# Kernel tuning notes

Hardware: AMD Instinct MI355X
Metric: run time of the kernel (lower is better)

The kernel has to match this reference:

```python
import jax, jax.numpy as jnp
import numpy as np


def setup_inputs() -> dict:
    key = jax.random.key(0)
    T, B, D, H = 512, 64, 512, 512
    k0, k1, k2, k3 = jax.random.split(key, 4)
    x = jax.random.normal(k0, (T, B, D), dtype=jnp.float32)
    # packed-sequence lengths, descending (as PackedSequence requires), at least T//2
    lengths = jnp.sort(jax.random.randint(k1, (B,), T // 2, T + 1))[::-1].astype(jnp.int64)
    s = 1.0 / np.sqrt(H)
    # gates stacked in order (i, f, c, o): same math as 8 separate per-gate linears
    Wx = jax.random.normal(k2, (4 * H, D), dtype=jnp.float32) * s
    Wh = jax.random.normal(k3, (4 * H, H), dtype=jnp.float32) * s
    # reset_parameters(): b_i = b_c = b_o = 0, b_f = 1
    b = jnp.concatenate([jnp.zeros(H), jnp.ones(H), jnp.zeros(2 * H)]).astype(jnp.float32)
    return {"x": x, "lengths": lengths, "Wx": Wx, "Wh": Wh, "b": b}


def reference(x, lengths, Wx, Wh, b):
    T, B, D = x.shape
    H = Wh.shape[1]
    # input projections for all timesteps at once (one big GEMM)
    xg = jnp.einsum('tbd,gd->tbg', x, Wx) + b  # [T, B, 4H]
    # validity mask per (t, b): packed recurrence only updates active rows
    mask = (jnp.arange(T)[:, None] < lengths[None, :])[..., None]  # [T, B, 1]

    def step(carry, inp):
        h, c = carry
        xg_t, m = inp
        g = xg_t + h @ Wh.T  # [B, 4H]
        i, f, cc, o = jnp.split(g, 4, axis=-1)
        i = jax.nn.sigmoid(i)
        f = jax.nn.sigmoid(f)
        o = jax.nn.sigmoid(o)
        c_t = f * c + i * jnp.tanh(cc)
        h_t = o * jnp.tanh(c_t)
        c_new = jnp.where(m, c_t, c)
        h_new = jnp.where(m, h_t, h)
        out_t = jnp.where(m, h_new, jnp.zeros((), x.dtype))
        return (h_new, c_new), out_t

    h0 = jnp.zeros((B, H), dtype=x.dtype)
    (h_T, c_T), out = jax.lax.scan(step, (h0, h0), (xg, mask))
    return out  # padded equivalent of the PackedSequence output, [T, B, H]
```

## Files before the change

kernel.cpp:

```cpp
#include <hip/hip_runtime.h>
#include <stdint.h>


#define TT 512
#define BB 64
#define DD 512
#define HH 512
#define NWG 256
#define NTHR 512
#define GR 8

typedef short short8 __attribute__((ext_vector_type(8)));
typedef float f32x4 __attribute__((ext_vector_type(4)));

__device__ __forceinline__ uint16_t bf16_rne(float f) {
  uint32_t u = __float_as_uint(f);
  u += 0x7fffu + ((u >> 16) & 1u);
  return (uint16_t)(u >> 16);
}

__device__ __forceinline__ void split2(float f, uint16_t &hi, uint16_t &lo) {
  uint16_t h = bf16_rne(f);
  hi = h;
  lo = bf16_rne(f - __uint_as_float(((uint32_t)h) << 16));
}

__device__ __forceinline__ float sigf(float v) { return 1.0f / (1.0f + __expf(-v)); }
__device__ __forceinline__ float tanh_(float v) {
  return 1.0f - 2.0f / (__expf(2.0f * v) + 1.0f);
}

__global__ void build_frags(const float* __restrict__ W, uint32_t* __restrict__ frag) {
  const int tid = blockIdx.x * 256 + threadIdx.x;
  const int lane = tid & 63;
  const int ks = (tid >> 6) & 15;
  const int nblk = tid >> 10;
  const int col = nblk * 16 + (lane & 15);
  const int k0 = ks * 32 + ((lane >> 4) << 3);
  const float* src = W + (size_t)col * 512 + k0;
  float4 a = *(const float4*)(src);
  float4 b = *(const float4*)(src + 4);
  float v[8] = {a.x, a.y, a.z, a.w, b.x, b.y, b.z, b.w};
  uint32_t hw[4], lw[4];
#pragma unroll
  for (int j = 0; j < 4; ++j) {
    uint16_t h0, l0, h1, l1;
    split2(v[2 * j], h0, l0);
    split2(v[2 * j + 1], h1, l1);
    hw[j] = (uint32_t)h0 | ((uint32_t)h1 << 16);
    lw[j] = (uint32_t)l0 | ((uint32_t)l1 << 16);
  }
  uint4* dst = (uint4*)(frag + (size_t)tid * 8);
  dst[0] = make_uint4(hw[0], hw[1], hw[2], hw[3]);
  dst[1] = make_uint4(lw[0], lw[1], lw[2], lw[3]);
}

__global__ __launch_bounds__(NTHR, 2) void lstm_main(
    const float* __restrict__ x, const int* __restrict__ len,
    const float* __restrict__ bias, const uint32_t* __restrict__ fragWx,
    const uint32_t* __restrict__ fragWh, uint32_t* __restrict__ h_pair,
    float* __restrict__ out) {
  const int tid = threadIdx.x;
  const int lane = tid & 63;
  const int wave = tid >> 6;
  const int gp = wave >> 1;
  const int kh = wave & 1;
  const int group = blockIdx.x & 7;
  const int jblk = blockIdx.x >> 3;
  const int b0 = group * GR;
  const int j0 = jblk << 4;
  uint32_t* hbase = h_pair + (size_t)group * 2 * (GR * HH);

  __shared__ uint16_t AH[GR * 512];
  __shared__ uint16_t AL[GR * 512];
  __shared__ float ex[8][GR][16];
  __shared__ float c_st[GR][16];
  __shared__ float h_st[GR][16];
  __shared__ float bias_l[4][16];
  __shared__ int len_l[GR];

  if (tid < GR * 16) {
    c_st[tid >> 4][tid & 15] = 0.0f;
    h_st[tid >> 4][tid & 15] = 0.0f;
  }
  if (tid < 64) bias_l[tid >> 4][tid & 15] = bias[(size_t)(tid >> 4) * HH + j0 + (tid & 15)];
  if (tid < GR) len_l[tid] = len[b0 + tid];

  short8 bxh[8], bxl[8], bhh[8], bhl[8];
  {
    const int nblk = gp * 32 + jblk;
#pragma unroll
    for (int ksl = 0; ksl < 8; ++ksl) {
      const size_t idx = ((size_t)(nblk * 16 + kh * 8 + ksl) * 64 + lane) * 8;
      uint4 vh = *(const uint4*)(fragWx + idx);
      uint4 vl = *(const uint4*)(fragWx + idx + 4);
      bxh[ksl] = __builtin_bit_cast(short8, vh);
      bxl[ksl] = __builtin_bit_cast(short8, vl);
      uint4 wh = *(const uint4*)(fragWh + idx);
      uint4 wl = *(const uint4*)(fragWh + idx + 4);
      bhh[ksl] = __builtin_bit_cast(short8, wh);
      bhl[ksl] = __builtin_bit_cast(short8, wl);
    }
  }

  const int arow = lane & 7;
  const int achk = (lane >> 4) << 4;
  const int axr = arow << 4;
  const char* rowH = (const char*)AH + arow * 1024;
  const char* rowL = (const char*)AL + arow * 1024;

  f32x4 hh = {0.f, 0.f, 0.f, 0.f}, lh = {0.f, 0.f, 0.f, 0.f}, hl = {0.f, 0.f, 0.f, 0.f};
  float4 xp[2];

#define LOAD_XP(tt)                                                            \
  _Pragma("unroll") for (int i = 0; i < 2; ++i) {                              \
    const int flat4 = i * 2048 + tid * 4;                                      \
    const int row = flat4 >> 9;                                                \
    const int col = flat4 & 511;                                               \
    xp[i] = *(const float4*)(x + ((size_t)(tt) * BB + b0 + row) * DD + col);   \
  }

#define STAGE_XP()                                                             \
  _Pragma("unroll") for (int i = 0; i < 2; ++i) {                              \
    const int flat4 = i * 2048 + tid * 4;                                      \
    const int row = flat4 >> 9;                                                \
    const int col = flat4 & 511;                                               \
    uint16_t h0, l0, h1, l1, h2, l2, h3, l3;                                   \
    split2(xp[i].x, h0, l0);                                                   \
    split2(xp[i].y, h1, l1);                                                   \
    split2(xp[i].z, h2, l2);                                                   \
    split2(xp[i].w, h3, l3);                                                   \
    const uint32_t hw0 = (uint32_t)h0 | ((uint32_t)h1 << 16);                  \
    const uint32_t hw1 = (uint32_t)h2 | ((uint32_t)h3 << 16);                  \
    const uint32_t lw0 = (uint32_t)l0 | ((uint32_t)l1 << 16);                  \
    const uint32_t lw1 = (uint32_t)l2 | ((uint32_t)l3 << 16);                  \
    const int off = row * 1024 + ((col * 2) ^ (row << 4));                     \
    *(uint2*)((char*)AH + off) = make_uint2(hw0, hw1);                         \
    *(uint2*)((char*)AL + off) = make_uint2(lw0, lw1);                         \
  }

#define X_MFMA()                                                               \
  hh = (f32x4){0.f, 0.f, 0.f, 0.f};                                           \
  lh = (f32x4){0.f, 0.f, 0.f, 0.f};                                           \
  hl = (f32x4){0.f, 0.f, 0.f, 0.f};                                           \
  _Pragma("unroll") for (int ksl = 0; ksl < 8; ++ksl) {                        \
    const int off = ((kh * 8 + ksl) * 64 + achk) ^ axr;                        \
    short8 ah = *(const short8*)(rowH + off);                                  \
    short8 al = *(const short8*)(rowL + off);                                  \
    hh = __builtin_amdgcn_mfma_f32_16x16x32_bf16(ah, bxh[ksl], hh, 0, 0, 0);   \
    lh = __builtin_amdgcn_mfma_f32_16x16x32_bf16(al, bxh[ksl], lh, 0, 0, 0);   \
    hl = __builtin_amdgcn_mfma_f32_16x16x32_bf16(ah, bxl[ksl], hl, 0, 0, 0);   \
  }

  LOAD_XP(0);
  __syncthreads();
  STAGE_XP();
  __syncthreads();
  X_MFMA();
  LOAD_XP(1);

  for (int t = 0; t < TT; ++t) {
    const int rbuf = t & 1;
    const int wbuf = rbuf ^ 1;

    if (t > 0) {
      const uint32_t tagp = (((uint32_t)(t - 1)) >> 1) & 3u;
      const uint32_t EXd = ((tagp & 1u) << 14) | ((tagp >> 1) << 30);
      const uint64_t EX2 = ((uint64_t)EXd << 32) | EXd;
      const uint64_t MK2 = 0x4000400040004000ull;
      const unsigned long long* pb =
          (const unsigned long long*)(hbase + (size_t)rbuf * (GR * HH)) +
          (size_t)tid * 4;
      uint64_t w0, w1, w2, w3;
      for (;;) {
        w0 = __hip_atomic_load(pb + 0, __ATOMIC_RELAXED, __HIP_MEMORY_SCOPE_AGENT);
        w1 = __hip_atomic_load(pb + 1, __ATOMIC_RELAXED, __HIP_MEMORY_SCOPE_AGENT);
        w2 = __hip_atomic_load(pb + 2, __ATOMIC_RELAXED, __HIP_MEMORY_SCOPE_AGENT);
        w3 = __hip_atomic_load(pb + 3, __ATOMIC_RELAXED, __HIP_MEMORY_SCOPE_AGENT);
        const uint64_t bad =
            (((w0 ^ EX2) | (w1 ^ EX2) | (w2 ^ EX2) | (w3 ^ EX2)) & MK2);
        if (bad == 0ull) break;
      }
      __syncthreads();

      {
        const uint32_t CM = ~0x40004000u;
        uint32_t d0 = (uint32_t)w0 & CM, d1 = (uint32_t)(w0 >> 32) & CM;
        uint32_t d2 = (uint32_t)w1 & CM, d3 = (uint32_t)(w1 >> 32) & CM;
        uint32_t d4 = (uint32_t)w2 & CM, d5 = (uint32_t)(w2 >> 32) & CM;
        uint32_t d6 = (uint32_t)w3 & CM, d7 = (uint32_t)(w3 >> 32) & CM;
        const uint32_t hi0 = (d0 & 0xFFFFu) | (d1 << 16);
        const uint32_t lo0 = (d0 >> 16) | (d1 & 0xFFFF0000u);
        const uint32_t hi1 = (d2 & 0xFFFFu) | (d3 << 16);
        const uint32_t lo1 = (d2 >> 16) | (d3 & 0xFFFF0000u);
        const uint32_t hi2 = (d4 & 0xFFFFu) | (d5 << 16);
        const uint32_t lo2 = (d4 >> 16) | (d5 & 0xFFFF0000u);
        const uint32_t hi3 = (d6 & 0xFFFFu) | (d7 << 16);
        const uint32_t lo3 = (d6 >> 16) | (d7 & 0xFFFF0000u);
        const int woff = wave * 1024 + ((lane * 16) ^ (wave << 4));
        *(uint4*)((char*)AH + woff) = make_uint4(hi0, hi1, hi2, hi3);
        *(uint4*)((char*)AL + woff) = make_uint4(lo0, lo1, lo2, lo3);
      }
      __syncthreads();

#pragma unroll
      for (int ksl = 0; ksl < 8; ++ksl) {
        const int off = ((kh * 8 + ksl) * 64 + achk) ^ axr;
        short8 ah = *(const short8*)(rowH + off);
        short8 al = *(const short8*)(rowL + off);
        hh = __builtin_amdgcn_mfma_f32_16x16x32_bf16(ah, bhh[ksl], hh, 0, 0, 0);
        lh = __builtin_amdgcn_mfma_f32_16x16x32_bf16(al, bhh[ksl], lh, 0, 0, 0);
        hl = __builtin_amdgcn_mfma_f32_16x16x32_bf16(ah, bhl[ksl], hl, 0, 0, 0);
      }
    }

    {
      const int crow = (lane >> 4) << 2;
      const int ccol = lane & 15;
      if (crow < GR) {
#pragma unroll
        for (int r = 0; r < 4; ++r) ex[wave][crow + r][ccol] = hh[r] + lh[r] + hl[r];
      }
    }
    __syncthreads();

    if (tid < GR * 16) {
      const int brow = tid >> 4;
      const int jc = tid & 15;
      const float p0 = ex[0][brow][jc] + ex[1][brow][jc] + bias_l[0][jc];
      const float p1 = ex[2][brow][jc] + ex[3][brow][jc] + bias_l[1][jc];
      const float p2 = ex[4][brow][jc] + ex[5][brow][jc] + bias_l[2][jc];
      const float p3 = ex[6][brow][jc] + ex[7][brow][jc] + bias_l[3][jc];
      const float ig = sigf(p0);
      const float fg = sigf(p1);
      const float cc = tanh_(p2);
      const float og = sigf(p3);
      const float co = c_st[brow][jc];
      const float ct = fg * co + ig * cc;
      const float ht = og * tanh_(ct);
      const bool m = (t < len_l[brow]);
      const float cn = m ? ct : co;
      const float hn = m ? ht : h_st[brow][jc];
      c_st[brow][jc] = cn;
      h_st[brow][jc] = hn;
      out[((size_t)t * BB + b0 + brow) * HH + j0 + jc] = m ? ht : 0.0f;
      uint16_t ph, pl;
      split2(hn, ph, pl);
      const uint32_t tagw = (((uint32_t)t) >> 1) & 3u;
      const uint32_t TB = ((tagw & 1u) << 14) | ((tagw >> 1) << 30);
      const uint32_t hv = ((uint32_t)ph | ((uint32_t)pl << 16)) | TB;
      __hip_atomic_store(hbase + (size_t)wbuf * (GR * HH) + brow * HH + j0 + jc,
                         hv, __ATOMIC_RELAXED, __HIP_MEMORY_SCOPE_AGENT);
    }

    if (t + 1 < TT) {
      STAGE_XP();
      __syncthreads();
      X_MFMA();
      LOAD_XP(min(t + 2, TT - 1));
    }
  }
}

extern "C" void kernel_launch(void* const* d_in, const int* in_sizes, int n_in,
                              void* d_out, int out_size, void* d_ws, size_t ws_size,
                              hipStream_t stream) {
  const float* x = (const float*)d_in[0];
  const int* len = (const int*)d_in[1];
  const float* Wx = (const float*)d_in[2];
  const float* Wh = (const float*)d_in[3];
  const float* bias = (const float*)d_in[4];
  float* out = (float*)d_out;

  const size_t FRAG_DW = (size_t)128 * 16 * 64 * 8;
  uint32_t* fragWx = (uint32_t*)d_ws;
  uint32_t* fragWh = fragWx + FRAG_DW;
  uint32_t* h_pair = fragWh + FRAG_DW;

  hipMemsetAsync(h_pair, 0xFF, (size_t)8 * 2 * GR * HH * 4, stream);

  build_frags<<<dim3(512), dim3(256), 0, stream>>>(Wx, fragWx);
  build_frags<<<dim3(512), dim3(256), 0, stream>>>(Wh, fragWh);

  void* args[] = {(void*)&x,      (void*)&len,    (void*)&bias, (void*)&fragWx,
                  (void*)&fragWh, (void*)&h_pair, (void*)&out};
  hipLaunchCooperativeKernel((void*)lstm_main, dim3(NWG), dim3(NTHR), args, 0, stream);
}
```

Before: 1.445 ms.

## Add workgroup-scope local h exchange buffer with fallback to agent-scope polling

Adds a second copy of the hidden-state exchange buffer that producers write with workgroup-scope atomic stores and that consumers poll using atomic fetch_add of zero. The idea is to hit a nearer cache level (same XCD/L2) instead of the agent-scope path. The local poll gets a bounded number of tries. If it never sees the expected tag, that workgroup falls back for good to the original agent-scope polling. This doubles the h stores, adds a memset, and relies on cross-workgroup visibility that workgroup scope does not guarantee, so correctness leans on the fallback.

```diff
diff --git a/kernel.cpp b/kernel.cpp
--- a/kernel.cpp
+++ b/kernel.cpp
@@ -59,7 +59,7 @@
     const float* __restrict__ x, const int* __restrict__ len,
     const float* __restrict__ bias, const uint32_t* __restrict__ fragWx,
     const uint32_t* __restrict__ fragWh, uint32_t* __restrict__ h_pair,
-    float* __restrict__ out) {
+    uint32_t* __restrict__ h_loc, float* __restrict__ out) {
   const int tid = threadIdx.x;
   const int lane = tid & 63;
   const int wave = tid >> 6;
@@ -70,6 +70,7 @@
   const int b0 = group * GR;
   const int j0 = jblk << 4;
   uint32_t* hbase = h_pair + (size_t)group * 2 * (GR * HH);
+  uint32_t* lbase = h_loc + (size_t)group * 2 * (GR * HH);
 
   __shared__ uint16_t AH[GR * 512];
   __shared__ uint16_t AL[GR * 512];
@@ -111,6 +112,7 @@
 
   f32x4 hh = {0.f, 0.f, 0.f, 0.f}, lh = {0.f, 0.f, 0.f, 0.f}, hl = {0.f, 0.f, 0.f, 0.f};
   float4 xp[2];
+  bool use_local = true;
 
 #define LOAD_XP(tt)                                                            \
   _Pragma("unroll") for (int i = 0; i < 2; ++i) {                              \
@@ -168,18 +170,42 @@
       const uint32_t EXd = ((tagp & 1u) << 14) | ((tagp >> 1) << 30);
       const uint64_t EX2 = ((uint64_t)EXd << 32) | EXd;
       const uint64_t MK2 = 0x4000400040004000ull;
-      const unsigned long long* pb =
-          (const unsigned long long*)(hbase + (size_t)rbuf * (GR * HH)) +
-          (size_t)tid * 4;
       uint64_t w0, w1, w2, w3;
-      for (;;) {
-        w0 = __hip_atomic_load(pb + 0, __ATOMIC_RELAXED, __HIP_MEMORY_SCOPE_AGENT);
-        w1 = __hip_atomic_load(pb + 1, __ATOMIC_RELAXED, __HIP_MEMORY_SCOPE_AGENT);
-        w2 = __hip_atomic_load(pb + 2, __ATOMIC_RELAXED, __HIP_MEMORY_SCOPE_AGENT);
-        w3 = __hip_atomic_load(pb + 3, __ATOMIC_RELAXED, __HIP_MEMORY_SCOPE_AGENT);
-        const uint64_t bad =
-            (((w0 ^ EX2) | (w1 ^ EX2) | (w2 ^ EX2) | (w3 ^ EX2)) & MK2);
-        if (bad == 0ull) break;
+      bool got = false;
+
+      if (use_local) {
+        unsigned long long* lp =
+            (unsigned long long*)(lbase + (size_t)rbuf * (GR * HH)) +
+            (size_t)tid * 4;
+        int tries = (t == 1) ? 256 : 16;
+        do {
+          w0 = __hip_atomic_fetch_add(lp + 0, 0ull, __ATOMIC_RELAXED,
+                                      __HIP_MEMORY_SCOPE_WORKGROUP);
+          w1 = __hip_atomic_fetch_add(lp + 1, 0ull, __ATOMIC_RELAXED,
+                                      __HIP_MEMORY_SCOPE_WORKGROUP);
+          w2 = __hip_atomic_fetch_add(lp + 2, 0ull, __ATOMIC_RELAXED,
+                                      __HIP_MEMORY_SCOPE_WORKGROUP);
+          w3 = __hip_atomic_fetch_add(lp + 3, 0ull, __ATOMIC_RELAXED,
+                                      __HIP_MEMORY_SCOPE_WORKGROUP);
+          got = ((((w0 ^ EX2) | (w1 ^ EX2) | (w2 ^ EX2) | (w3 ^ EX2)) & MK2) ==
+                 0ull);
+        } while (!got && --tries);
+        if (!got) use_local = false;
+      }
+
+      if (!got) {
+        const unsigned long long* pb =
+            (const unsigned long long*)(hbase + (size_t)rbuf * (GR * HH)) +
+            (size_t)tid * 4;
+        for (;;) {
+          w0 = __hip_atomic_load(pb + 0, __ATOMIC_RELAXED, __HIP_MEMORY_SCOPE_AGENT);
+          w1 = __hip_atomic_load(pb + 1, __ATOMIC_RELAXED, __HIP_MEMORY_SCOPE_AGENT);
+          w2 = __hip_atomic_load(pb + 2, __ATOMIC_RELAXED, __HIP_MEMORY_SCOPE_AGENT);
+          w3 = __hip_atomic_load(pb + 3, __ATOMIC_RELAXED, __HIP_MEMORY_SCOPE_AGENT);
+          const uint64_t bad =
+              (((w0 ^ EX2) | (w1 ^ EX2) | (w2 ^ EX2) | (w3 ^ EX2)) & MK2);
+          if (bad == 0ull) break;
+        }
       }
       __syncthreads();
 
@@ -249,8 +275,11 @@
       const uint32_t tagw = (((uint32_t)t) >> 1) & 3u;
       const uint32_t TB = ((tagw & 1u) << 14) | ((tagw >> 1) << 30);
       const uint32_t hv = ((uint32_t)ph | ((uint32_t)pl << 16)) | TB;
-      __hip_atomic_store(hbase + (size_t)wbuf * (GR * HH) + brow * HH + j0 + jc,
-                         hv, __ATOMIC_RELAXED, __HIP_MEMORY_SCOPE_AGENT);
+      const size_t eoff = (size_t)wbuf * (GR * HH) + brow * HH + j0 + jc;
+      __hip_atomic_store(lbase + eoff, hv, __ATOMIC_RELAXED,
+                         __HIP_MEMORY_SCOPE_WORKGROUP);
+      __hip_atomic_store(hbase + eoff, hv, __ATOMIC_RELAXED,
+                         __HIP_MEMORY_SCOPE_AGENT);
     }
 
     if (t + 1 < TT) {
@@ -273,16 +302,19 @@
   float* out = (float*)d_out;
 
   const size_t FRAG_DW = (size_t)128 * 16 * 64 * 8;
+  const size_t HP_DW = (size_t)8 * 2 * GR * HH;
   uint32_t* fragWx = (uint32_t*)d_ws;
   uint32_t* fragWh = fragWx + FRAG_DW;
   uint32_t* h_pair = fragWh + FRAG_DW;
-
-  hipMemsetAsync(h_pair, 0xFF, (size_t)8 * 2 * GR * HH * 4, stream);
+  uint32_t* h_loc = h_pair + HP_DW;
+
+  hipMemsetAsync(h_pair, 0xFF, HP_DW * 4, stream);
+  hipMemsetAsync(h_loc, 0xFF, HP_DW * 4, stream);
 
   build_frags<<<dim3(512), dim3(256), 0, stream>>>(Wx, fragWx);
   build_frags<<<dim3(512), dim3(256), 0, stream>>>(Wh, fragWh);
 
-  void* args[] = {(void*)&x,      (void*)&len,    (void*)&bias, (void*)&fragWx,
-                  (void*)&fragWh, (void*)&h_pair, (void*)&out};
+  void* args[] = {(void*)&x,      (void*)&len,   (void*)&bias, (void*)&fragWx,
+                  (void*)&fragWh, (void*)&h_pair, (void*)&h_loc, (void*)&out};
   hipLaunchCooperativeKernel((void*)lstm_main, dim3(NWG), dim3(NTHR), args, 0, stream);
 }
```

Measured after the change: 1.585 ms. 1.1x slower.

## Hoist input projection into separate GEMM kernel and halve recurrent workgroups

Applied to the files above, without the earlier changes.

Moves the x·Wx input projection out of the serial recurrence into a separate parallel GEMM kernel that writes a [T,B,4H] fp32 buffer to workspace. The recurrent kernel then only does the h·Wh MFMAs and prefetches the precomputed gate inputs, with 16 batch rows per group across 128 workgroups instead of 8 rows across 256. This takes work off the latency-bound critical path and reduces the number of communicating workgroups. In exchange it needs an extra 256MB-class workspace write/read, and falls back to the old kernel if the workspace is too small.

```diff
diff --git a/kernel.cpp b/kernel.cpp
--- a/kernel.cpp
+++ b/kernel.cpp
@@ -6,9 +6,11 @@
 #define BB 64
 #define DD 512
 #define HH 512
-#define NWG 256
 #define NTHR 512
-#define GR 8
+#define NWG2 128
+#define GR2 16
+#define NWG4 256
+#define GR4 8
 
 typedef short short8 __attribute__((ext_vector_type(8)));
 typedef float f32x4 __attribute__((ext_vector_type(4)));
@@ -55,62 +57,244 @@
   dst[1] = make_uint4(lw[0], lw[1], lw[2], lw[3]);
 }
 
-__global__ __launch_bounds__(NTHR, 2) void lstm_main(
-    const float* __restrict__ x, const int* __restrict__ len,
-    const float* __restrict__ bias, const uint32_t* __restrict__ fragWx,
-    const uint32_t* __restrict__ fragWh, uint32_t* __restrict__ h_pair,
+__global__ __launch_bounds__(NTHR, 1) void xg_gemm(
+    const float* __restrict__ x, const float* __restrict__ bias,
+    const uint32_t* __restrict__ fragWx, float* __restrict__ xg) {
+  const int t = blockIdx.x;
+  const int tid = threadIdx.x;
+  const int lane = tid & 63;
+  const int wave = tid >> 6;
+  const int gate = wave & 3;
+  const int jsub = wave >> 2;
+
+  __shared__ uint16_t AH[64 * 512];
+  __shared__ uint16_t AL[64 * 512];
+
+#pragma unroll
+  for (int i = 0; i < 16; ++i) {
+    const int flat4 = i * 2048 + tid * 4;
+    const int row = flat4 >> 9;
+    const int col = flat4 & 511;
+    float4 v = *(const float4*)(x + ((size_t)t * BB + row) * DD + col);
+    uint16_t h0, l0, h1, l1, h2, l2, h3, l3;
+    split2(v.x, h0, l0);
+    split2(v.y, h1, l1);
+    split2(v.z, h2, l2);
+    split2(v.w, h3, l3);
+    const int off = row * 1024 + ((col * 2) ^ ((row & 7) << 4));
+    *(uint2*)((char*)AH + off) =
+        make_uint2((uint32_t)h0 | ((uint32_t)h1 << 16), (uint32_t)h2 | ((uint32_t)h3 << 16));
+    *(uint2*)((char*)AL + off) =
+        make_uint2((uint32_t)l0 | ((uint32_t)l1 << 16), (uint32_t)l2 | ((uint32_t)l3 << 16));
+  }
+  __syncthreads();
+
+  const int achk = (lane >> 4) << 4;
+  const int axr = (lane & 7) << 4;
+
+  for (int jp = 0; jp < 16; ++jp) {
+    const int jblk = jp * 2 + jsub;
+    const int nblk = gate * 32 + jblk;
+    short8 bh[16], bl[16];
+#pragma unroll
+    for (int ks = 0; ks < 16; ++ks) {
+      const size_t idx = ((size_t)(nblk * 16 + ks) * 64 + lane) * 8;
+      bh[ks] = __builtin_bit_cast(short8, *(const uint4*)(fragWx + idx));
+      bl[ks] = __builtin_bit_cast(short8, *(const uint4*)(fragWx + idx + 4));
+    }
+    const int colg = (nblk << 4) + (lane & 15);
+    const float bv = bias[colg];
+    for (int m = 0; m < 4; ++m) {
+      const char* rowH = (const char*)AH + (m * 16 + (lane & 15)) * 1024;
+      const char* rowL = (const char*)AL + (m * 16 + (lane & 15)) * 1024;
+      f32x4 hh = {0.f, 0.f, 0.f, 0.f}, lh = {0.f, 0.f, 0.f, 0.f}, hl = {0.f, 0.f, 0.f, 0.f};
+#pragma unroll
+      for (int ks = 0; ks < 16; ++ks) {
+        const int off = (ks * 64 + achk) ^ axr;
+        short8 ah = *(const short8*)(rowH + off);
+        short8 al = *(const short8*)(rowL + off);
+        hh = __builtin_amdgcn_mfma_f32_16x16x32_bf16(ah, bh[ks], hh, 0, 0, 0);
+        lh = __builtin_amdgcn_mfma_f32_16x16x32_bf16(al, bh[ks], lh, 0, 0, 0);
+        hl = __builtin_amdgcn_mfma_f32_16x16x32_bf16(ah, bl[ks], hl, 0, 0, 0);
+      }
+      const int r0 = m * 16 + ((lane >> 4) << 2);
+#pragma unroll
+      for (int i = 0; i < 4; ++i)
+        xg[((size_t)t * BB + r0 + i) * 2048 + colg] = hh[i] + lh[i] + hl[i] + bv;
+    }
+  }
+}
+
+__global__ __launch_bounds__(NTHR, 2) void lstm2(
+    const int* __restrict__ len, const uint32_t* __restrict__ fragWh,
+    const float* __restrict__ xg, uint32_t* __restrict__ h_pair,
     float* __restrict__ out) {
   const int tid = threadIdx.x;
   const int lane = tid & 63;
   const int wave = tid >> 6;
   const int gp = wave >> 1;
   const int kh = wave & 1;
-  const int group = blockIdx.x & 7;
-  const int jblk = blockIdx.x >> 3;
-  const int b0 = group * GR;
+  const int group = blockIdx.x & 3;
+  const int jblk = blockIdx.x >> 2;
+  const int b0 = group * GR2;
   const int j0 = jblk << 4;
-  uint32_t* hbase = h_pair + (size_t)group * 2 * (GR * HH);
-
-  __shared__ uint16_t AH[GR * 512];
-  __shared__ uint16_t AL[GR * 512];
-  __shared__ float ex[8][GR][16];
-  __shared__ float c_st[GR][16];
-  __shared__ float h_st[GR][16];
-  __shared__ float bias_l[4][16];
-  __shared__ int len_l[GR];
-
-  if (tid < GR * 16) {
+  uint32_t* hbase = h_pair + (size_t)group * 2 * (GR2 * HH);
+
+  __shared__ uint16_t AH[GR2 * 512];
+  __shared__ uint16_t AL[GR2 * 512];
+  __shared__ float ex[8][GR2][16];
+  __shared__ float c_st[GR2][16];
+  __shared__ float h_st[GR2][16];
+  __shared__ int len_l[GR2];
+
+  if (tid < GR2 * 16) {
     c_st[tid >> 4][tid & 15] = 0.0f;
     h_st[tid >> 4][tid & 15] = 0.0f;
   }
-  if (tid < 64) bias_l[tid >> 4][tid & 15] = bias[(size_t)(tid >> 4) * HH + j0 + (tid & 15)];
-  if (tid < GR) len_l[tid] = len[b0 + tid];
-
-  short8 bxh[8], bxl[8], bhh[8], bhl[8];
+  if (tid < GR2) len_l[tid] = len[b0 + tid];
+
+  short8 bhh[8], bhl[8];
   {
     const int nblk = gp * 32 + jblk;
 #pragma unroll
     for (int ksl = 0; ksl < 8; ++ksl) {
       const size_t idx = ((size_t)(nblk * 16 + kh * 8 + ksl) * 64 + lane) * 8;
-      uint4 vh = *(const uint4*)(fragWx + idx);
-      uint4 vl = *(const uint4*)(fragWx + idx + 4);
-      bxh[ksl] = __builtin_bit_cast(short8, vh);
-      bxl[ksl] = __builtin_bit_cast(short8, vl);
-      uint4 wh = *(const uint4*)(fragWh + idx);
-      uint4 wl = *(const uint4*)(fragWh + idx + 4);
-      bhh[ksl] = __builtin_bit_cast(short8, wh);
-      bhl[ksl] = __builtin_bit_cast(short8, wl);
-    }
-  }
-
-  const int arow = lane & 7;
+      bhh[ksl] = __builtin_bit_cast(short8, *(const uint4*)(fragWh + idx));
+      bhl[ksl] = __builtin_bit_cast(short8, *(const uint4*)(fragWh + idx + 4));
+    }
+  }
+
+  const int arow = lane & 15;
   const int achk = (lane >> 4) << 4;
-  const int axr = arow << 4;
+  const int axr = (arow & 7) << 4;
   const char* rowH = (const char*)AH + arow * 1024;
   const char* rowL = (const char*)AL + arow * 1024;
 
-  f32x4 hh = {0.f, 0.f, 0.f, 0.f}, lh = {0.f, 0.f, 0.f, 0.f}, hl = {0.f, 0.f, 0.f, 0.f};
-  float4 xp[2];
+  const int brow = tid >> 4;
+  const int jc = tid & 15;
+
+  float xc0 = 0.f, xc1 = 0.f, xc2 = 0.f, xc3 = 0.f;
+  float xn0 = 0.f, xn1 = 0.f, xn2 = 0.f, xn3 = 0.f;
+  if (tid < 256) {
+    const size_t xb = ((size_t)b0 + brow) * 2048 + j0 + jc;
+    xc0 = xg[xb];
+    xc1 = xg[xb + 512];
+    xc2 = xg[xb + 1024];
+    xc3 = xg[xb + 1536];
+  }
+
+  for (int t = 0; t < TT; ++t) {
+    const int rbuf = t & 1;
+    const int wbuf = rbuf ^ 1;
+
+    if (tid < 256) {
+      const int tn = (t + 1 < TT) ? t + 1 : t;
+      const size_t xb = ((size_t)tn * BB + b0 + brow) * 2048 + j0 + jc;
+      xn0 = xg[xb];
+      xn1 = xg[xb + 512];
+      xn2 = xg[xb + 1024];
+      xn3 = xg[xb + 1536];
+    }
+
+    f32x4 hh = {0.f, 0.f, 0.f, 0.f}, lh = {0.f, 0.f, 0.f, 0.f}, hl = {0.f, 0.f, 0.f, 0.f};
+
+    if (t > 0) {
+      const uint32_t tagp = (((uint32_t)(t - 1)) >> 1) & 3u;
+      const uint32_t EXd = ((tagp & 1u) << 14) | ((tagp >> 1) << 30);
+      const uint64_t EX2 = ((uint64_t)EXd << 32) | EXd;
+      const uint64_t MK2 = 0x4000400040004000ull;
+      const unsigned long long* pb =
+          (const unsigned long long*)(hbase + (size_t)rbuf * (GR2 * HH)) +
+          (size_t)tid * 8;
+      uint64_t w[8];
+      for (;;) {
+#pragma unroll
+        for (int q = 0; q < 8; ++q)
+          w[q] = __hip_atomic_load(pb + q, __ATOMIC_RELAXED, __HIP_MEMORY_SCOPE_AGENT);
+        uint64_t bad = 0;
+#pragma unroll
+        for (int q = 0; q < 8; ++q) bad |= (w[q] ^ EX2);
+        if ((bad & MK2) == 0ull) break;
+      }
+
+      {
+        const uint32_t CM = ~0x40004000u;
+        uint32_t d[16];
+#pragma unroll
+        for (int q = 0; q < 8; ++q) {
+          d[2 * q] = (uint32_t)w[q] & CM;
+          d[2 * q + 1] = (uint32_t)(w[q] >> 32) & CM;
+        }
+        uint32_t hw[8], lw[8];
+#pragma unroll
+        for (int j = 0; j < 8; ++j) {
+          hw[j] = (d[2 * j] & 0xFFFFu) | (d[2 * j + 1] << 16);
+          lw[j] = (d[2 * j] >> 16) | (d[2 * j + 1] & 0xFFFF0000u);
+        }
+        const int rrow = tid >> 5;
+        const int colb = (tid & 31) * 32;
+        const int base = rrow * 1024;
+        const int swz = (rrow & 7) << 4;
+        *(uint4*)((char*)AH + base + (colb ^ swz)) = make_uint4(hw[0], hw[1], hw[2], hw[3]);
+        *(uint4*)((char*)AH + base + ((colb + 16) ^ swz)) = make_uint4(hw[4], hw[5], hw[6], hw[7]);
+        *(uint4*)((char*)AL + base + (colb ^ swz)) = make_uint4(lw[0], lw[1], lw[2], lw[3]);
+        *(uint4*)((char*)AL + base + ((colb + 16) ^ swz)) = make_uint4(lw[4], lw[5], lw[6], lw[7]);
+      }
+    }
+    __syncthreads();
+
+    if (t > 0) {
+#pragma unroll
+      for (int ksl = 0; ksl < 8; ++ksl) {
+        const int off = ((kh * 8 + ksl) * 64 + achk) ^ axr;
+        short8 ah = *(const short8*)(rowH + off);
+        short8 al = *(const short8*)(rowL + off);
+        hh = __builtin_amdgcn_mfma_f32_16x16x32_bf16(ah, bhh[ksl], hh, 0, 0, 0);
+        lh = __builtin_amdgcn_mfma_f32_16x16x32_bf16(al, bhh[ksl], lh, 0, 0, 0);
+        hl = __builtin_amdgcn_mfma_f32_16x16x32_bf16(ah, bhl[ksl], hl, 0, 0, 0);
+      }
+    }
+
+    {
+      const int crow = (lane >> 4) << 2;
+      const int ccol = lane & 15;
+#pragma unroll
+      for (int r = 0; r < 4; ++r) ex[wave][crow + r][ccol] = hh[r] + lh[r] + hl[r];
+    }
+    __syncthreads();
+
+    if (tid < 256) {
+      const float p0 = ex[0][brow][jc] + ex[1][brow][jc] + xc0;
+      const float p1 = ex[2][brow][jc] + ex[3][brow][jc] + xc1;
+      const float p2 = ex[4][brow][jc] + ex[5][brow][jc] + xc2;
+      const float p3 = ex[6][brow][jc] + ex[7][brow][jc] + xc3;
+      const float ig = sigf(p0);
+      const float fg = sigf(p1);
+      const float cc = tanh_(p2);
+      const float og = sigf(p3);
+      const float co = c_st[brow][jc];
+      const float ct = fg * co + ig * cc;
+      const float ht = og * tanh_(ct);
+      const bool m = (t < len_l[brow]);
+      const float cn = m ? ct : co;
+      const float hn = m ? ht : h_st[brow][jc];
+      c_st[brow][jc] = cn;
+      h_st[brow][jc] = hn;
+      out[((size_t)t * BB + b0 + brow) * HH + j0 + jc] = m ? ht : 0.0f;
+      uint16_t ph, pl;
+      split2(hn, ph, pl);
+      const uint32_t tagw = (((uint32_t)t) >> 1) & 3u;
+      const uint32_t TB = ((tagw & 1u) << 14) | ((tagw >> 1) << 30);
+      __hip_atomic_store(hbase + (size_t)wbuf * (GR2 * HH) + brow * HH + j0 + jc,
+                         ((uint32_t)ph | ((uint32_t)pl << 16)) | TB,
+                         __ATOMIC_RELAXED, __HIP_MEMORY_SCOPE_AGENT);
+      xc0 = xn0;
+      xc1 = xn1;
+      xc2 = xn2;
+      xc3 = xn3;
+    }
+  }
+}
 
 #define LOAD_XP(tt)                                                            \
   _Pragma("unroll") for (int i = 0; i < 2; ++i) {                              \
@@ -152,6 +336,59 @@
     hl = __builtin_amdgcn_mfma_f32_16x16x32_bf16(ah, bxl[ksl], hl, 0, 0, 0);   \
   }
 
+__global__ __launch_bounds__(NTHR, 2) void lstm_r4(
+    const float* __restrict__ x, const int* __restrict__ len,
+    const float* __restrict__ bias, const uint32_t* __restrict__ fragWx,
+    const uint32_t* __restrict__ fragWh, uint32_t* __restrict__ h_pair,
+    float* __restrict__ out) {
+  const int tid = threadIdx.x;
+  const int lane = tid & 63;
+  const int wave = tid >> 6;
+  const int gp = wave >> 1;
+  const int kh = wave & 1;
+  const int group = blockIdx.x & 7;
+  const int jblk = blockIdx.x >> 3;
+  const int b0 = group * GR4;
+  const int j0 = jblk << 4;
+  uint32_t* hbase = h_pair + (size_t)group * 2 * (GR4 * HH);
+
+  __shared__ uint16_t AH[GR4 * 512];
+  __shared__ uint16_t AL[GR4 * 512];
+  __shared__ float ex[8][GR4][16];
+  __shared__ float c_st[GR4][16];
+  __shared__ float h_st[GR4][16];
+  __shared__ float bias_l[4][16];
+  __shared__ int len_l[GR4];
+
+  if (tid < GR4 * 16) {
+    c_st[tid >> 4][tid & 15] = 0.0f;
+    h_st[tid >> 4][tid & 15] = 0.0f;
+  }
+  if (tid < 64) bias_l[tid >> 4][tid & 15] = bias[(size_t)(tid >> 4) * HH + j0 + (tid & 15)];
+  if (tid < GR4) len_l[tid] = len[b0 + tid];
+
+  short8 bxh[8], bxl[8], bhh[8], bhl[8];
+  {
+    const int nblk = gp * 32 + jblk;
+#pragma unroll
+    for (int ksl = 0; ksl < 8; ++ksl) {
+      const size_t idx = ((size_t)(nblk * 16 + kh * 8 + ksl) * 64 + lane) * 8;
+      bxh[ksl] = __builtin_bit_cast(short8, *(const uint4*)(fragWx + idx));
+      bxl[ksl] = __builtin_bit_cast(short8, *(const uint4*)(fragWx + idx + 4));
+      bhh[ksl] = __builtin_bit_cast(short8, *(const uint4*)(fragWh + idx));
+      bhl[ksl] = __builtin_bit_cast(short8, *(const uint4*)(fragWh + idx + 4));
+    }
+  }
+
+  const int arow = lane & 7;
+  const int achk = (lane >> 4) << 4;
+  const int axr = arow << 4;
+  const char* rowH = (const char*)AH + arow * 1024;
+  const char* rowL = (const char*)AL + arow * 1024;
+
+  f32x4 hh = {0.f, 0.f, 0.f, 0.f}, lh = {0.f, 0.f, 0.f, 0.f}, hl = {0.f, 0.f, 0.f, 0.f};
+  float4 xp[2];
+
   LOAD_XP(0);
   __syncthreads();
   STAGE_XP();
@@ -169,7 +406,7 @@
       const uint64_t EX2 = ((uint64_t)EXd << 32) | EXd;
       const uint64_t MK2 = 0x4000400040004000ull;
       const unsigned long long* pb =
-          (const unsigned long long*)(hbase + (size_t)rbuf * (GR * HH)) +
+          (const unsigned long long*)(hbase + (size_t)rbuf * (GR4 * HH)) +
           (size_t)tid * 4;
       uint64_t w0, w1, w2, w3;
       for (;;) {
@@ -217,14 +454,14 @@
     {
       const int crow = (lane >> 4) << 2;
       const int ccol = lane & 15;
-      if (crow < GR) {
+      if (crow < GR4) {
 #pragma unroll
         for (int r = 0; r < 4; ++r) ex[wave][crow + r][ccol] = hh[r] + lh[r] + hl[r];
       }
     }
     __syncthreads();
 
-    if (tid < GR * 16) {
+    if (tid < GR4 * 16) {
       const int brow = tid >> 4;
       const int jc = tid & 15;
       const float p0 = ex[0][brow][jc] + ex[1][brow][jc] + bias_l[0][jc];
@@ -249,7 +486,7 @@
       const uint32_t tagw = (((uint32_t)t) >> 1) & 3u;
       const uint32_t TB = ((tagw & 1u) << 14) | ((tagw >> 1) << 30);
       const uint32_t hv = ((uint32_t)ph | ((uint32_t)pl << 16)) | TB;
-      __hip_atomic_store(hbase + (size_t)wbuf * (GR * HH) + brow * HH + j0 + jc,
+      __hip_atomic_store(hbase + (size_t)wbuf * (GR4 * HH) + brow * HH + j0 + jc,
                          hv, __ATOMIC_RELAXED, __HIP_MEMORY_SCOPE_AGENT);
     }
 
@@ -261,6 +498,9 @@
     }
   }
 }
+#undef LOAD_XP
+#undef STAGE_XP
+#undef X_MFMA
 
 extern "C" void kernel_launch(void* const* d_in, const int* in_sizes, int n_in,
                               void* d_out, int out_size, void* d_ws, size_t ws_size,
@@ -273,16 +513,27 @@
   float* out = (float*)d_out;
 
   const size_t FRAG_DW = (size_t)128 * 16 * 64 * 8;
+  const size_t HP_DW = 65536;
+  const size_t XG_DW = (size_t)TT * BB * 2048;
   uint32_t* fragWx = (uint32_t*)d_ws;
   uint32_t* fragWh = fragWx + FRAG_DW;
   uint32_t* h_pair = fragWh + FRAG_DW;
-
-  hipMemsetAsync(h_pair, 0xFF, (size_t)8 * 2 * GR * HH * 4, stream);
+  float* xg = (float*)(h_pair + HP_DW);
+  const size_t need = (2 * FRAG_DW + HP_DW + XG_DW) * 4;
+
+  hipMemsetAsync(h_pair, 0xFF, HP_DW * 4, stream);
 
   build_frags<<<dim3(512), dim3(256), 0, stream>>>(Wx, fragWx);
   build_frags<<<dim3(512), dim3(256), 0, stream>>>(Wh, fragWh);
 
-  void* args[] = {(void*)&x,      (void*)&len,    (void*)&bias, (void*)&fragWx,
-                  (void*)&fragWh, (void*)&h_pair, (void*)&out};
-  hipLaunchCooperativeKernel((void*)lstm_main, dim3(NWG), dim3(NTHR), args, 0, stream);
-}
+  if (ws_size >= need) {
+    xg_gemm<<<dim3(TT), dim3(NTHR), 0, stream>>>(x, bias, fragWx, xg);
+    void* args[] = {(void*)&len, (void*)&fragWh, (void*)&xg, (void*)&h_pair,
+                    (void*)&out};
+    hipLaunchCooperativeKernel((void*)lstm2, dim3(NWG2), dim3(NTHR), args, 0, stream);
+  } else {
+    void* args[] = {(void*)&x,      (void*)&len,    (void*)&bias, (void*)&fragWx,
+                    (void*)&fragWh, (void*)&h_pair, (void*)&out};
+    hipLaunchCooperativeKernel((void*)lstm_r4, dim3(NWG4), dim3(NTHR), args, 0, stream);
+  }
+}
```

Result: no change. 1.439 ms (-0.4%).

## Split workgroup into hidden and input wave teams with 16-row batch groups

Applied to the files above, without the earlier changes.

Halves the workgroup count by giving each workgroup 16 batch rows instead of 8. Waves are specialized: four waves do the recurrent h·Wh MFMA, one gate each over full K, and four waves compute the x·Wx projection for the next timestep into a triple-buffered LDS area, synchronized through LDS-counter team barriers. The goal is to take the input projection off the serial recurrence critical path and cut the cross-workgroup spin traffic. The cost is more per-thread polling loads (16 per thread) and more LDS use, and a fragile custom barrier scheme.

```diff
diff --git a/kernel.cpp b/kernel.cpp
--- a/kernel.cpp
+++ b/kernel.cpp
@@ -6,9 +6,9 @@
 #define BB 64
 #define DD 512
 #define HH 512
-#define NWG 256
+#define NWG 128
 #define NTHR 512
-#define GR 8
+#define GR 16
 
 typedef short short8 __attribute__((ext_vector_type(8)));
 typedef float f32x4 __attribute__((ext_vector_type(4)));
@@ -55,7 +55,7 @@
   dst[1] = make_uint4(lw[0], lw[1], lw[2], lw[3]);
 }
 
-__global__ __launch_bounds__(NTHR, 2) void lstm_main(
+__global__ __launch_bounds__(NTHR, 2) void lstm4(
     const float* __restrict__ x, const int* __restrict__ len,
     const float* __restrict__ bias, const uint32_t* __restrict__ fragWx,
     const uint32_t* __restrict__ fragWh, uint32_t* __restrict__ h_pair,
@@ -63,174 +63,217 @@
   const int tid = threadIdx.x;
   const int lane = tid & 63;
   const int wave = tid >> 6;
-  const int gp = wave >> 1;
-  const int kh = wave & 1;
-  const int group = blockIdx.x & 7;
-  const int jblk = blockIdx.x >> 3;
+  const bool isH = wave < 4;
+  const int gate = wave & 3;
+  const int group = blockIdx.x & 3;
+  const int jblk = blockIdx.x >> 2;
   const int b0 = group * GR;
   const int j0 = jblk << 4;
   uint32_t* hbase = h_pair + (size_t)group * 2 * (GR * HH);
 
   __shared__ uint16_t AH[GR * 512];
   __shared__ uint16_t AL[GR * 512];
-  __shared__ float ex[8][GR][16];
+  __shared__ uint16_t XH[GR * 512];
+  __shared__ uint16_t XL[GR * 512];
+  __shared__ float ex_x[3][4][GR][16];
+  __shared__ float ex_h[2][4][GR][16];
   __shared__ float c_st[GR][16];
   __shared__ float h_st[GR][16];
   __shared__ float bias_l[4][16];
   __shared__ int len_l[GR];
-
-  if (tid < GR * 16) {
+  __shared__ uint32_t tb[2];
+
+  if (tid == 0) { tb[0] = 0u; tb[1] = 0u; }
+  if (tid < 256) {
     c_st[tid >> 4][tid & 15] = 0.0f;
     h_st[tid >> 4][tid & 15] = 0.0f;
   }
   if (tid < 64) bias_l[tid >> 4][tid & 15] = bias[(size_t)(tid >> 4) * HH + j0 + (tid & 15)];
   if (tid < GR) len_l[tid] = len[b0 + tid];
 
-  short8 bxh[8], bxl[8], bhh[8], bhl[8];
+  short8 wfh[16], wfl[16];
   {
-    const int nblk = gp * 32 + jblk;
-#pragma unroll
-    for (int ksl = 0; ksl < 8; ++ksl) {
-      const size_t idx = ((size_t)(nblk * 16 + kh * 8 + ksl) * 64 + lane) * 8;
-      uint4 vh = *(const uint4*)(fragWx + idx);
-      uint4 vl = *(const uint4*)(fragWx + idx + 4);
-      bxh[ksl] = __builtin_bit_cast(short8, vh);
-      bxl[ksl] = __builtin_bit_cast(short8, vl);
-      uint4 wh = *(const uint4*)(fragWh + idx);
-      uint4 wl = *(const uint4*)(fragWh + idx + 4);
-      bhh[ksl] = __builtin_bit_cast(short8, wh);
-      bhl[ksl] = __builtin_bit_cast(short8, wl);
+    const uint32_t* fw = isH ? fragWh : fragWx;
+    const int nblk = gate * 32 + jblk;
+#pragma unroll
+    for (int ks = 0; ks < 16; ++ks) {
+      const size_t idx = ((size_t)(nblk * 16 + ks) * 64 + lane) * 8;
+      wfh[ks] = __builtin_bit_cast(short8, *(const uint4*)(fw + idx));
+      wfl[ks] = __builtin_bit_cast(short8, *(const uint4*)(fw + idx + 4));
     }
   }
 
-  const int arow = lane & 7;
+  const int arow = lane & 15;
   const int achk = (lane >> 4) << 4;
-  const int axr = arow << 4;
-  const char* rowH = (const char*)AH + arow * 1024;
-  const char* rowL = (const char*)AL + arow * 1024;
-
-  f32x4 hh = {0.f, 0.f, 0.f, 0.f}, lh = {0.f, 0.f, 0.f, 0.f}, hl = {0.f, 0.f, 0.f, 0.f};
-  float4 xp[2];
-
-#define LOAD_XP(tt)                                                            \
-  _Pragma("unroll") for (int i = 0; i < 2; ++i) {                              \
-    const int flat4 = i * 2048 + tid * 4;                                      \
-    const int row = flat4 >> 9;                                                \
-    const int col = flat4 & 511;                                               \
-    xp[i] = *(const float4*)(x + ((size_t)(tt) * BB + b0 + row) * DD + col);   \
-  }
-
-#define STAGE_XP()                                                             \
-  _Pragma("unroll") for (int i = 0; i < 2; ++i) {                              \
-    const int flat4 = i * 2048 + tid * 4;                                      \
-    const int row = flat4 >> 9;                                                \
-    const int col = flat4 & 511;                                               \
-    uint16_t h0, l0, h1, l1, h2, l2, h3, l3;                                   \
-    split2(xp[i].x, h0, l0);                                                   \
-    split2(xp[i].y, h1, l1);                                                   \
-    split2(xp[i].z, h2, l2);                                                   \
-    split2(xp[i].w, h3, l3);                                                   \
-    const uint32_t hw0 = (uint32_t)h0 | ((uint32_t)h1 << 16);                  \
-    const uint32_t hw1 = (uint32_t)h2 | ((uint32_t)h3 << 16);                  \
-    const uint32_t lw0 = (uint32_t)l0 | ((uint32_t)l1 << 16);                  \
-    const uint32_t lw1 = (uint32_t)l2 | ((uint32_t)l3 << 16);                  \
-    const int off = row * 1024 + ((col * 2) ^ (row << 4));                     \
-    *(uint2*)((char*)AH + off) = make_uint2(hw0, hw1);                         \
-    *(uint2*)((char*)AL + off) = make_uint2(lw0, lw1);                         \
-  }
-
-#define X_MFMA()                                                               \
-  hh = (f32x4){0.f, 0.f, 0.f, 0.f};                                           \
-  lh = (f32x4){0.f, 0.f, 0.f, 0.f};                                           \
-  hl = (f32x4){0.f, 0.f, 0.f, 0.f};                                           \
-  _Pragma("unroll") for (int ksl = 0; ksl < 8; ++ksl) {                        \
-    const int off = ((kh * 8 + ksl) * 64 + achk) ^ axr;                        \
-    short8 ah = *(const short8*)(rowH + off);                                  \
-    short8 al = *(const short8*)(rowL + off);                                  \
-    hh = __builtin_amdgcn_mfma_f32_16x16x32_bf16(ah, bxh[ksl], hh, 0, 0, 0);   \
-    lh = __builtin_amdgcn_mfma_f32_16x16x32_bf16(al, bxh[ksl], lh, 0, 0, 0);   \
-    hl = __builtin_amdgcn_mfma_f32_16x16x32_bf16(ah, bxl[ksl], hl, 0, 0, 0);   \
-  }
-
-  LOAD_XP(0);
+  const int axr = (arow & 7) << 4;
+
+  const uint64_t MK2 = 0x4000400040004000ull;
+  const uint32_t CM = ~0x40004000u;
+
   __syncthreads();
-  STAGE_XP();
-  __syncthreads();
-  X_MFMA();
-  LOAD_XP(1);
+
+  uint32_t btgt = 0;
+#define TEAM_BAR(IDX)                                                          \
+  {                                                                            \
+    btgt += 4;                                                                 \
+    if (lane == 0)                                                             \
+      __hip_atomic_fetch_add(&tb[IDX], 1u, __ATOMIC_ACQ_REL,                   \
+                             __HIP_MEMORY_SCOPE_WORKGROUP);                    \
+    while (__hip_atomic_load(&tb[IDX], __ATOMIC_ACQUIRE,                       \
+                             __HIP_MEMORY_SCOPE_WORKGROUP) < btgt) {}          \
+    asm volatile("" ::: "memory");                                             \
+  }
+
+  float4 xp[8];
+#define XLOAD(tt)                                                              \
+  {                                                                            \
+    const int xid = tid - 256;                                                 \
+    _Pragma("unroll") for (int i = 0; i < 8; ++i) {                            \
+      const int f4 = i * 1024 + xid * 4;                                       \
+      const int row = f4 >> 9;                                                 \
+      const int col = f4 & 511;                                                \
+      xp[i] = *(const float4*)(x + ((size_t)(tt) * BB + b0 + row) * DD + col); \
+    }                                                                          \
+  }
+#define XSTAGE()                                                               \
+  {                                                                            \
+    const int xid = tid - 256;                                                 \
+    _Pragma("unroll") for (int i = 0; i < 8; ++i) {                            \
+      const int f4 = i * 1024 + xid * 4;                                       \
+      const int row = f4 >> 9;                                                 \
+      const int col = f4 & 511;                                                \
+      uint16_t h0, l0, h1, l1, h2, l2, h3, l3;                                 \
+      split2(xp[i].x, h0, l0);                                                 \
+      split2(xp[i].y, h1, l1);                                                 \
+      split2(xp[i].z, h2, l2);                                                 \
+      split2(xp[i].w, h3, l3);                                                 \
+      const int off = row * 1024 + ((col * 2) ^ ((row & 7) << 4));             \
+      *(uint2*)((char*)XH + off) = make_uint2(                                 \
+          (uint32_t)h0 | ((uint32_t)h1 << 16), (uint32_t)h2 | ((uint32_t)h3 << 16)); \
+      *(uint2*)((char*)XL + off) = make_uint2(                                 \
+          (uint32_t)l0 | ((uint32_t)l1 << 16), (uint32_t)l2 | ((uint32_t)l3 << 16)); \
+    }                                                                          \
+  }
+#define XMFMA(BUF)                                                             \
+  {                                                                            \
+    f32x4 hh = {0.f, 0.f, 0.f, 0.f}, lh = {0.f, 0.f, 0.f, 0.f},               \
+          hl = {0.f, 0.f, 0.f, 0.f};                                           \
+    const char* rH = (const char*)XH + arow * 1024;                            \
+    const char* rL = (const char*)XL + arow * 1024;                            \
+    _Pragma("unroll") for (int ks = 0; ks < 16; ++ks) {                        \
+      const int off = (ks * 64 + achk) ^ axr;                                  \
+      short8 ah = *(const short8*)(rH + off);                                  \
+      short8 al = *(const short8*)(rL + off);                                  \
+      hh = __builtin_amdgcn_mfma_f32_16x16x32_bf16(ah, wfh[ks], hh, 0, 0, 0);  \
+      lh = __builtin_amdgcn_mfma_f32_16x16x32_bf16(al, wfh[ks], lh, 0, 0, 0);  \
+      hl = __builtin_amdgcn_mfma_f32_16x16x32_bf16(ah, wfl[ks], hl, 0, 0, 0);  \
+    }                                                                          \
+    const int crow = (lane >> 4) << 2;                                         \
+    const int ccol = lane & 15;                                                \
+    _Pragma("unroll") for (int r = 0; r < 4; ++r)                              \
+      ex_x[BUF][gate][crow + r][ccol] =                                        \
+          hh[r] + lh[r] + hl[r] + bias_l[gate][ccol];                          \
+  }
+
+  if (!isH) {
+    XLOAD(0);
+    XSTAGE();
+    TEAM_BAR(1);
+    XMFMA(0);
+    XLOAD(1);
+  }
 
   for (int t = 0; t < TT; ++t) {
-    const int rbuf = t & 1;
-    const int wbuf = rbuf ^ 1;
-
-    if (t > 0) {
-      const uint32_t tagp = (((uint32_t)(t - 1)) >> 1) & 3u;
-      const uint32_t EXd = ((tagp & 1u) << 14) | ((tagp >> 1) << 30);
-      const uint64_t EX2 = ((uint64_t)EXd << 32) | EXd;
-      const uint64_t MK2 = 0x4000400040004000ull;
-      const unsigned long long* pb =
-          (const unsigned long long*)(hbase + (size_t)rbuf * (GR * HH)) +
-          (size_t)tid * 4;
-      uint64_t w0, w1, w2, w3;
-      for (;;) {
-        w0 = __hip_atomic_load(pb + 0, __ATOMIC_RELAXED, __HIP_MEMORY_SCOPE_AGENT);
-        w1 = __hip_atomic_load(pb + 1, __ATOMIC_RELAXED, __HIP_MEMORY_SCOPE_AGENT);
-        w2 = __hip_atomic_load(pb + 2, __ATOMIC_RELAXED, __HIP_MEMORY_SCOPE_AGENT);
-        w3 = __hip_atomic_load(pb + 3, __ATOMIC_RELAXED, __HIP_MEMORY_SCOPE_AGENT);
-        const uint64_t bad =
-            (((w0 ^ EX2) | (w1 ^ EX2) | (w2 ^ EX2) | (w3 ^ EX2)) & MK2);
-        if (bad == 0ull) break;
+    if (isH) {
+      if (t > 0) {
+        const int rbuf = t & 1;
+        const uint32_t tg = (((uint32_t)(t - 1)) >> 1) & 3u;
+        const uint32_t EXd = ((tg & 1u) << 14) | ((tg >> 1) << 30);
+        const uint64_t EX2 = ((uint64_t)EXd << 32) | EXd;
+        const unsigned long long* pb =
+            (const unsigned long long*)(hbase + (size_t)rbuf * (GR * HH)) +
+            (tid >> 4) * 256 + (tid & 15) * 16;
+        uint64_t w[16];
+        for (;;) {
+#pragma unroll
+          for (int q = 0; q < 16; ++q)
+            w[q] = __hip_atomic_load(pb + q, __ATOMIC_RELAXED, __HIP_MEMORY_SCOPE_AGENT);
+          uint64_t bad = 0;
+#pragma unroll
+          for (int q = 0; q < 16; ++q) bad |= (w[q] ^ EX2);
+          if ((bad & MK2) == 0ull) break;
+        }
+        {
+          const int base = (tid >> 4) * 1024;
+          const int swz = ((tid >> 4) & 7) << 4;
+          const int cb = (tid & 15) * 64;
+#pragma unroll
+          for (int c = 0; c < 4; ++c) {
+            const uint32_t d0 = (uint32_t)w[4 * c + 0] & CM;
+            const uint32_t d1 = (uint32_t)(w[4 * c + 0] >> 32) & CM;
+            const uint32_t d2 = (uint32_t)w[4 * c + 1] & CM;
+            const uint32_t d3 = (uint32_t)(w[4 * c + 1] >> 32) & CM;
+            const uint32_t d4 = (uint32_t)w[4 * c + 2] & CM;
+            const uint32_t d5 = (uint32_t)(w[4 * c + 2] >> 32) & CM;
+            const uint32_t d6 = (uint32_t)w[4 * c + 3] & CM;
+            const uint32_t d7 = (uint32_t)(w[4 * c + 3] >> 32) & CM;
+            const int off = base + ((cb + 16 * c) ^ swz);
+            *(uint4*)((char*)AH + off) = make_uint4(
+                (d0 & 0xFFFFu) | (d1 << 16), (d2 & 0xFFFFu) | (d3 << 16),
+                (d4 & 0xFFFFu) | (d5 << 16), (d6 & 0xFFFFu) | (d7 << 16));
+            *(uint4*)((char*)AL + off) = make_uint4(
+                (d0 >> 16) | (d1 & 0xFFFF0000u), (d2 >> 16) | (d3 & 0xFFFF0000u),
+                (d4 >> 16) | (d5 & 0xFFFF0000u), (d6 >> 16) | (d7 & 0xFFFF0000u));
+          }
+        }
+        TEAM_BAR(0);
+        {
+          f32x4 hh = {0.f, 0.f, 0.f, 0.f}, lh = {0.f, 0.f, 0.f, 0.f},
+                hl = {0.f, 0.f, 0.f, 0.f};
+          const char* rH = (const char*)AH + arow * 1024;
+          const char* rL = (const char*)AL + arow * 1024;
+#pragma unroll
+          for (int ks = 0; ks < 16; ++ks) {
+            const int off = (ks * 64 + achk) ^ axr;
+            short8 ah = *(const short8*)(rH + off);
+            short8 al = *(const short8*)(rL + off);
+            hh = __builtin_amdgcn_mfma_f32_16x16x32_bf16(ah, wfh[ks], hh, 0, 0, 0);
+            lh = __builtin_amdgcn_mfma_f32_16x16x32_bf16(al, wfh[ks], lh, 0, 0, 0);
+            hl = __builtin_amdgcn_mfma_f32_16x16x32_bf16(ah, wfl[ks], hl, 0, 0, 0);
+          }
+          const int crow = (lane >> 4) << 2;
+          const int ccol = lane & 15;
+#pragma unroll
+          for (int r = 0; r < 4; ++r)
+            ex_h[t & 1][gate][crow + r][ccol] = hh[r] + lh[r] + hl[r];
+        }
       }
-      __syncthreads();
-
-      {
-        const uint32_t CM = ~0x40004000u;
-        uint32_t d0 = (uint32_t)w0 & CM, d1 = (uint32_t)(w0 >> 32) & CM;
-        uint32_t d2 = (uint32_t)w1 & CM, d3 = (uint32_t)(w1 >> 32) & CM;
-        uint32_t d4 = (uint32_t)w2 & CM, d5 = (uint32_t)(w2 >> 32) & CM;
-        uint32_t d6 = (uint32_t)w3 & CM, d7 = (uint32_t)(w3 >> 32) & CM;
-        const uint32_t hi0 = (d0 & 0xFFFFu) | (d1 << 16);
-        const uint32_t lo0 = (d0 >> 16) | (d1 & 0xFFFF0000u);
-        const uint32_t hi1 = (d2 & 0xFFFFu) | (d3 << 16);
-        const uint32_t lo1 = (d2 >> 16) | (d3 & 0xFFFF0000u);
-        const uint32_t hi2 = (d4 & 0xFFFFu) | (d5 << 16);
-        const uint32_t lo2 = (d4 >> 16) | (d5 & 0xFFFF0000u);
-        const uint32_t hi3 = (d6 & 0xFFFFu) | (d7 << 16);
-        const uint32_t lo3 = (d6 >> 16) | (d7 & 0xFFFF0000u);
-        const int woff = wave * 1024 + ((lane * 16) ^ (wave << 4));
-        *(uint4*)((char*)AH + woff) = make_uint4(hi0, hi1, hi2, hi3);
-        *(uint4*)((char*)AL + woff) = make_uint4(lo0, lo1, lo2, lo3);
-      }
-      __syncthreads();
-
-#pragma unroll
-      for (int ksl = 0; ksl < 8; ++ksl) {
-        const int off = ((kh * 8 + ksl) * 64 + achk) ^ axr;
-        short8 ah = *(const short8*)(rowH + off);
-        short8 al = *(const short8*)(rowL + off);
-        hh = __builtin_amdgcn_mfma_f32_16x16x32_bf16(ah, bhh[ksl], hh, 0, 0, 0);
-        lh = __builtin_amdgcn_mfma_f32_16x16x32_bf16(al, bhh[ksl], lh, 0, 0, 0);
-        hl = __builtin_amdgcn_mfma_f32_16x16x32_bf16(ah, bhl[ksl], hl, 0, 0, 0);
+    } else {
+      if (t + 1 < TT) {
+        XSTAGE();
+        XLOAD(t + 2 < TT ? t + 2 : TT - 1);
+        TEAM_BAR(1);
+        XMFMA((t + 1) % 3);
       }
     }
 
-    {
-      const int crow = (lane >> 4) << 2;
-      const int ccol = lane & 15;
-      if (crow < GR) {
-#pragma unroll
-        for (int r = 0; r < 4; ++r) ex[wave][crow + r][ccol] = hh[r] + lh[r] + hl[r];
-      }
-    }
     __syncthreads();
 
-    if (tid < GR * 16) {
+    if (isH && tid < 256) {
       const int brow = tid >> 4;
       const int jc = tid & 15;
-      const float p0 = ex[0][brow][jc] + ex[1][brow][jc] + bias_l[0][jc];
-      const float p1 = ex[2][brow][jc] + ex[3][brow][jc] + bias_l[1][jc];
-      const float p2 = ex[4][brow][jc] + ex[5][brow][jc] + bias_l[2][jc];
-      const float p3 = ex[6][brow][jc] + ex[7][brow][jc] + bias_l[3][jc];
+      const int xb = t % 3;
+      float p0 = ex_x[xb][0][brow][jc];
+      float p1 = ex_x[xb][1][brow][jc];
+      float p2 = ex_x[xb][2][brow][jc];
+      float p3 = ex_x[xb][3][brow][jc];
+      if (t > 0) {
+        const int hb = t & 1;
+        p0 += ex_h[hb][0][brow][jc];
+        p1 += ex_h[hb][1][brow][jc];
+        p2 += ex_h[hb][2][brow][jc];
+        p3 += ex_h[hb][3][brow][jc];
+      }
       const float ig = sigf(p0);
       const float fg = sigf(p1);
       const float cc = tanh_(p2);
@@ -248,18 +291,15 @@
       split2(hn, ph, pl);
       const uint32_t tagw = (((uint32_t)t) >> 1) & 3u;
       const uint32_t TB = ((tagw & 1u) << 14) | ((tagw >> 1) << 30);
-      const uint32_t hv = ((uint32_t)ph | ((uint32_t)pl << 16)) | TB;
-      __hip_atomic_store(hbase + (size_t)wbuf * (GR * HH) + brow * HH + j0 + jc,
-                         hv, __ATOMIC_RELAXED, __HIP_MEMORY_SCOPE_AGENT);
+      __hip_atomic_store(hbase + (size_t)((t + 1) & 1) * (GR * HH) + brow * HH + j0 + jc,
+                         ((uint32_t)ph | ((uint32_t)pl << 16)) | TB,
+                         __ATOMIC_RELAXED, __HIP_MEMORY_SCOPE_AGENT);
     }
-
-    if (t + 1 < TT) {
-      STAGE_XP();
-      __syncthreads();
-      X_MFMA();
-      LOAD_XP(min(t + 2, TT - 1));
-    }
-  }
+  }
+#undef TEAM_BAR
+#undef XLOAD
+#undef XSTAGE
+#undef XMFMA
 }
 
 extern "C" void kernel_launch(void* const* d_in, const int* in_sizes, int n_in,
@@ -273,16 +313,17 @@
   float* out = (float*)d_out;
 
   const size_t FRAG_DW = (size_t)128 * 16 * 64 * 8;
+  const size_t HP_DW = (size_t)4 * 2 * GR * HH;
   uint32_t* fragWx = (uint32_t*)d_ws;
   uint32_t* fragWh = fragWx + FRAG_DW;
   uint32_t* h_pair = fragWh + FRAG_DW;
 
-  hipMemsetAsync(h_pair, 0xFF, (size_t)8 * 2 * GR * HH * 4, stream);
+  hipMemsetAsync(h_pair, 0xFF, HP_DW * 4, stream);
 
   build_frags<<<dim3(512), dim3(256), 0, stream>>>(Wx, fragWx);
   build_frags<<<dim3(512), dim3(256), 0, stream>>>(Wh, fragWh);
 
   void* args[] = {(void*)&x,      (void*)&len,    (void*)&bias, (void*)&fragWx,
                   (void*)&fragWh, (void*)&h_pair, (void*)&out};
-  hipLaunchCooperativeKernel((void*)lstm_main, dim3(NWG), dim3(NTHR), args, 0, stream);
-}
+  hipLaunchCooperativeKernel((void*)lstm4, dim3(NWG), dim3(NTHR), args, 0, stream);
+}
```

Measured after the change: 3.012 ms. 108% more time.
